# Kernel optimization log

Hardware: AMD Instinct MI355X
Metric: run time of the kernel (lower is better)

The kernel has to match this reference:

```python
import jax, jax.numpy as jnp
import numpy as np

B, T, E, H = 4, 2048, 1024, 16
D = E // H  # head dim = 64


def setup_inputs() -> dict:
    key = jax.random.key(0)
    k1, k2, k3 = jax.random.split(key, 3)
    g = jax.random.normal(k1, (B, T, E), dtype=jnp.float32)
    W_lift = jax.random.normal(k2, (2 * E, E), dtype=jnp.float32) * (1.0 / np.sqrt(E))
    W_proj = jax.random.normal(k3, (H, H), dtype=jnp.float32) * (1.0 / np.sqrt(H))
    return {"g": g, "W_lift": W_lift, "W_proj": W_proj}


def reference(g, W_lift, W_proj):
    b, t, e = g.shape
    h, d = H, e // H
    # lift: Linear(E, 2E, bias=False) -> split into q, k
    qk = jnp.einsum('bte,fe->btf', g, W_lift)  # (B, T, 2E)
    q, k = qk[..., :e], qk[..., e:]
    q = q.reshape(b, t, h, d).transpose(0, 2, 1, 3)  # (B, H, T, D)
    k = k.reshape(b, t, h, d).transpose(0, 2, 1, 3)  # (B, H, T, D)
    # unscaled causal scores
    a = jnp.einsum('bhqd,bhkd->bhqk', q, k)  # (B, H, T, T)
    causal = jnp.tril(jnp.ones((t, t), dtype=bool))
    a = jnp.where(causal[None, None], a, -jnp.inf)
    # masked logsumexp over key dim -> (B, H, T)
    lse = jax.scipy.special.logsumexp(a, axis=-1)
    out = lse.transpose(0, 2, 1)  # (B, T, H)
    out = jnp.einsum('bth,gh->btg', out, W_proj)  # proj Linear(H, H)
    out = out.sum(axis=2)  # (B, T)
    return out.reshape(-1, out.shape[-1])
```

## Files before the change

kernel.cpp:

```cpp
#include <hip/hip_runtime.h>
#include <hip/hip_bf16.h>

#define B_ 4
#define T_ 2048
#define E_ 1024
#define H_ 16
#define D_ 64
#define Mtot 8192
#define N2 2048
#define K_ 1024
#define PS_ (B_ * H_ * T_)
#define NKT 16
#define LOG2E 1.4426950408889634f

typedef __attribute__((ext_vector_type(8))) short short8;
typedef __attribute__((ext_vector_type(4))) float f32x4;
using bf16 = __hip_bfloat16;

__device__ __forceinline__ void async_copy16(const void* g, void* l) {
  __builtin_amdgcn_global_load_lds(
      (const __attribute__((address_space(1))) unsigned int*)g,
      (__attribute__((address_space(3))) unsigned int*)l, 16, 0, 0);
}

__global__ void cast_f32_to_bf16(const float* __restrict__ in, ushort* __restrict__ out, int n4) {
  int stride = gridDim.x * blockDim.x;
  for (int i = blockIdx.x * blockDim.x + threadIdx.x; i < n4; i += stride) {
    float4 v = reinterpret_cast<const float4*>(in)[i];
    bf16 a = __float2bfloat16(v.x), b = __float2bfloat16(v.y);
    bf16 c = __float2bfloat16(v.z), d = __float2bfloat16(v.w);
    ushort4 o = make_ushort4(*(ushort*)&a, *(ushort*)&b, *(ushort*)&c, *(ushort*)&d);
    reinterpret_cast<ushort4*>(out)[i] = o;
  }
}

#define MFMA_BF16(a, b, c) __builtin_amdgcn_mfma_f32_16x16x32_bf16(a, b, c, 0, 0, 0)

__launch_bounds__(512, 2)
__global__ void lift_gemm(const bf16* __restrict__ A, const bf16* __restrict__ Bm,
                          bf16* __restrict__ qh, bf16* __restrict__ kh) {
  __shared__ __align__(16) char sL[8][16384];
  const int bid = blockIdx.x;
  const int swz = ((bid & 7) << 5) | (bid >> 3);
  const int m0 = (swz >> 3) * 256;
  const int n0 = (swz & 7) * 256;
  const int tid = threadIdx.x;
  const int lane = tid & 63, w = tid >> 6;
  const int wm = w >> 2, wn = w & 3;
  const int lr = lane & 15, lg = lane >> 4;

  f32x4 acc[8][4];
#pragma unroll
  for (int i = 0; i < 8; ++i)
#pragma unroll
    for (int j = 0; j < 4; ++j) acc[i][j] = (f32x4)(0.0f);

  auto stage_half = [&](int slot, const bf16* gsrc, int Rbase, int kcol) {
#pragma unroll
    for (int it = 0; it < 2; ++it) {
      const int o = ((it * 512 + tid) << 4);
      const int lin = o ^ (((o >> 7) & 7) << 4);
      const int r = lin >> 7, cb = lin & 127;
      async_copy16((const char*)gsrc + ((size_t)(Rbase + r) * K_ + kcol) * 2 + cb,
                   &sL[slot][o]);
    }
  };
  auto rd = [&](int slot, int row, int khalf) -> short8 {
    int off = (row << 7) + (khalf << 6) + (lg << 4);
    off ^= (row & 7) << 4;
    return *(const short8*)&sL[slot][off];
  };

  stage_half(0, A, m0, 0);
  stage_half(1, A, m0 + 128, 0);
  stage_half(2, Bm, n0, 0);
  stage_half(3, Bm, n0 + 128, 0);

  short8 af[4][2], bf0[2][2], bf1[2][2];

  for (int kt = 0; kt < NKT; ++kt) {
    const int cb = (kt & 1) << 2;
    const int nb = cb ^ 4;
    const int kcol = (kt + 1) * 64;
    const int aslot = cb + wm;
    const int bslot = cb + 2 + (wn >> 1);
    const int brow = (wn & 1) * 64;

    if (kt + 1 < NKT) {
      stage_half(nb + 0, A, m0, kcol);
      stage_half(nb + 1, A, m0 + 128, kcol);
      asm volatile("s_waitcnt vmcnt(4)" ::: "memory");
    } else {
      asm volatile("s_waitcnt vmcnt(0)" ::: "memory");
    }
    __builtin_amdgcn_sched_barrier(0);
    __builtin_amdgcn_s_barrier();
#pragma unroll
    for (int i = 0; i < 4; ++i) {
      af[i][0] = rd(aslot, i * 16 + lr, 0);
      af[i][1] = rd(aslot, i * 16 + lr, 1);
    }
#pragma unroll
    for (int j = 0; j < 2; ++j) {
      bf0[j][0] = rd(bslot, brow + j * 16 + lr, 0);
      bf0[j][1] = rd(bslot, brow + j * 16 + lr, 1);
    }
    __builtin_amdgcn_s_setprio(1);
#pragma unroll
    for (int i = 0; i < 4; ++i)
#pragma unroll
      for (int j = 0; j < 2; ++j) {
        acc[i][j] = MFMA_BF16(af[i][0], bf0[j][0], acc[i][j]);
        acc[i][j] = MFMA_BF16(af[i][1], bf0[j][1], acc[i][j]);
      }
    __builtin_amdgcn_s_setprio(0);
    __builtin_amdgcn_sched_barrier(0);
    __builtin_amdgcn_s_barrier();

    if (kt + 1 < NKT) {
      stage_half(nb + 2, Bm, n0, kcol);
      stage_half(nb + 3, Bm, n0 + 128, kcol);
    }
#pragma unroll
    for (int j = 0; j < 2; ++j) {
      bf1[j][0] = rd(bslot, brow + (j + 2) * 16 + lr, 0);
      bf1[j][1] = rd(bslot, brow + (j + 2) * 16 + lr, 1);
    }
    __builtin_amdgcn_sched_barrier(0);
    __builtin_amdgcn_s_barrier();
    __builtin_amdgcn_s_setprio(1);
#pragma unroll
    for (int i = 0; i < 4; ++i)
#pragma unroll
      for (int j = 0; j < 2; ++j) {
        acc[i][j + 2] = MFMA_BF16(af[i][0], bf1[j][0], acc[i][j + 2]);
        acc[i][j + 2] = MFMA_BF16(af[i][1], bf1[j][1], acc[i][j + 2]);
      }
    __builtin_amdgcn_s_setprio(0);
    __builtin_amdgcn_sched_barrier(0);
    __builtin_amdgcn_s_barrier();

#pragma unroll
    for (int i = 0; i < 4; ++i) {
      af[i][0] = rd(aslot, (i + 4) * 16 + lr, 0);
      af[i][1] = rd(aslot, (i + 4) * 16 + lr, 1);
    }
    __builtin_amdgcn_sched_barrier(0);
    __builtin_amdgcn_s_barrier();
    __builtin_amdgcn_s_setprio(1);
#pragma unroll
    for (int i = 0; i < 4; ++i)
#pragma unroll
      for (int j = 0; j < 2; ++j) {
        acc[i + 4][j] = MFMA_BF16(af[i][0], bf0[j][0], acc[i + 4][j]);
        acc[i + 4][j] = MFMA_BF16(af[i][1], bf0[j][1], acc[i + 4][j]);
      }
    __builtin_amdgcn_s_setprio(0);
    __builtin_amdgcn_sched_barrier(0);
    __builtin_amdgcn_s_barrier();

    __builtin_amdgcn_s_setprio(1);
#pragma unroll
    for (int i = 0; i < 4; ++i)
#pragma unroll
      for (int j = 0; j < 2; ++j) {
        acc[i + 4][j + 2] = MFMA_BF16(af[i][0], bf1[j][0], acc[i + 4][j + 2]);
        acc[i + 4][j + 2] = MFMA_BF16(af[i][1], bf1[j][1], acc[i + 4][j + 2]);
      }
    __builtin_amdgcn_s_setprio(0);
    __builtin_amdgcn_sched_barrier(0);
    __builtin_amdgcn_s_barrier();
  }

  const float qscale = (n0 < E_) ? LOG2E : 1.0f;
#pragma unroll
  for (int mi = 0; mi < 8; ++mi) {
#pragma unroll
    for (int ni = 0; ni < 4; ++ni) {
#pragma unroll
      for (int r = 0; r < 4; ++r) {
        int m = m0 + wm * 128 + mi * 16 + lg * 4 + r;
        int f = n0 + wn * 64 + ni * 16 + lr;
        bf16 bv = __float2bfloat16(acc[mi][ni][r] * qscale);
        int b = m >> 11, t = m & (T_ - 1);
        int hh = (f & (E_ - 1)) >> 6, d = f & (D_ - 1);
        bf16* dst = (f < E_) ? qh : kh;
        dst[((((size_t)b * H_ + hh) * T_) + t) * D_ + d] = bv;
      }
    }
  }
}

#define LSE_QT 128

__launch_bounds__(256)
__global__ void attn_lse(const bf16* __restrict__ qh, const bf16* __restrict__ kh,
                         float* __restrict__ psum) {
  __shared__ __align__(16) char sK[2][8192];
  const int bid = blockIdx.x;
  const int qt = 15 - (bid >> 8);
  const int rem = bid & 255;
  const int bh = rem >> 2;
  const int s = rem & 3;
  const int tid = threadIdx.x;
  const int lane = tid & 63, w = tid >> 6;
  const int lr = lane & 15, lg = lane >> 4;
  const int qbase = qt * LSE_QT + w * 32;

  const bf16* qp = qh + ((size_t)bh * T_ + qbase) * D_;
  short8 qf[2][2];
#pragma unroll
  for (int f = 0; f < 2; ++f)
#pragma unroll
    for (int h = 0; h < 2; ++h)
      qf[f][h] = *(const short8*)&qp[(size_t)(f * 16 + lr) * D_ + h * 32 + lg * 8];

  float l[2][4];
#pragma unroll
  for (int f = 0; f < 2; ++f)
#pragma unroll
    for (int r = 0; r < 4; ++r) l[f][r] = 0.0f;

  const char* kbase = (const char*)(kh + (size_t)bh * T_ * D_);
  const int nfullw = qbase >> 6;
  const int maxk = 2 * qt + 1;
  const int nt = (s <= maxk) ? ((maxk - s) >> 2) + 1 : 0;

#define STAGE_K(bi, kt_)                                                      \
  do {                                                                        \
    const char* kp_ = kbase + (size_t)(kt_) * (64 * D_ * 2);                  \
    _Pragma("unroll") for (int it = 0; it < 2; ++it) {                        \
      const int o = ((w * 2 + it) << 10) | (lane << 4);                       \
      const int lin = o ^ (((o >> 7) & 7) << 4);                              \
      async_copy16(kp_ + lin, (char*)&sK[bi][0] + ((w * 2 + it) << 10));      \
    }                                                                         \
  } while (0)

  auto krd = [&](const char* kb, int row, int khalf) -> short8 {
    int off = (row << 7) + (khalf << 6) + (lg << 4);
    off ^= (row & 7) << 4;
    return *(const short8*)(kb + off);
  };

  int cur = 0;
  if (nt > 0) STAGE_K(0, s);
  for (int i = 0; i < nt; ++i) {
    if (i + 1 < nt) {
      STAGE_K(cur ^ 1, s + 4 * (i + 1));
      asm volatile("s_waitcnt vmcnt(2)" ::: "memory");
    } else {
      asm volatile("s_waitcnt vmcnt(0)" ::: "memory");
    }
    __builtin_amdgcn_sched_barrier(0);
    __builtin_amdgcn_s_barrier();

    const int kt = s + 4 * i;
    if (kt <= nfullw) {
      const char* kb = &sK[cur][0];
      short8 kf[4][2];
#pragma unroll
      for (int j = 0; j < 4; ++j) {
        kf[j][0] = krd(kb, j * 16 + lr, 0);
        kf[j][1] = krd(kb, j * 16 + lr, 1);
      }
      f32x4 sc[2][4];
#pragma unroll
      for (int f = 0; f < 2; ++f)
#pragma unroll
        for (int j = 0; j < 4; ++j) sc[f][j] = (f32x4)(0.0f);
#pragma unroll
      for (int j = 0; j < 4; ++j) {
        sc[0][j] = MFMA_BF16(qf[0][0], kf[j][0], sc[0][j]);
        sc[0][j] = MFMA_BF16(qf[0][1], kf[j][1], sc[0][j]);
        sc[1][j] = MFMA_BF16(qf[1][0], kf[j][0], sc[1][j]);
        sc[1][j] = MFMA_BF16(qf[1][1], kf[j][1], sc[1][j]);
      }
      if (kt < nfullw) {
#pragma unroll
        for (int f = 0; f < 2; ++f)
#pragma unroll
          for (int j = 0; j < 4; ++j)
#pragma unroll
            for (int r = 0; r < 4; ++r)
              l[f][r] += __builtin_amdgcn_exp2f(sc[f][j][r]);
      } else {
#pragma unroll
        for (int f = 0; f < 2; ++f)
#pragma unroll
          for (int j = 0; j < 4; ++j)
#pragma unroll
            for (int r = 0; r < 4; ++r) {
              int qrow = qbase + f * 16 + lg * 4 + r;
              int key = kt * 64 + j * 16 + lr;
              float a = (key <= qrow) ? sc[f][j][r] : -INFINITY;
              l[f][r] += __builtin_amdgcn_exp2f(a);
            }
      }
    }
    __builtin_amdgcn_sched_barrier(0);
    __builtin_amdgcn_s_barrier();
    cur ^= 1;
  }

#pragma unroll
  for (int f = 0; f < 2; ++f)
#pragma unroll
    for (int r = 0; r < 4; ++r) {
      float v = l[f][r];
      v += __shfl_xor(v, 1);
      v += __shfl_xor(v, 2);
      v += __shfl_xor(v, 4);
      v += __shfl_xor(v, 8);
      if (lr == 0)
        psum[(size_t)s * PS_ + (size_t)bh * T_ + qbase + f * 16 + lg * 4 + r] = v;
    }
}

__global__ void proj_out(const float* __restrict__ psum, const float* __restrict__ Wp,
                         float* __restrict__ out) {
  __shared__ float cw[H_];
  int tid = threadIdx.x;
  if (tid < H_) {
    float s = 0.0f;
    for (int g = 0; g < H_; ++g) s += Wp[g * H_ + tid];
    cw[tid] = s;
  }
  __syncthreads();
  int idx = blockIdx.x * blockDim.x + tid;
  int b = idx >> 11, t = idx & (T_ - 1);
  float acc = 0.0f;
#pragma unroll
  for (int h = 0; h < H_; ++h) {
    size_t base = ((size_t)(b * H_ + h) * T_) + t;
    float v = psum[base] + psum[PS_ + base] + psum[2 * (size_t)PS_ + base] +
              psum[3 * (size_t)PS_ + base];
    acc += __logf(v) * cw[h];
  }
  out[idx] = acc;
}

extern "C" void kernel_launch(void* const* d_in, const int* in_sizes, int n_in,
                              void* d_out, int out_size, void* d_ws, size_t ws_size,
                              hipStream_t stream) {
  (void)in_sizes; (void)n_in; (void)out_size; (void)ws_size;
  const float* g  = (const float*)d_in[0];
  const float* Wl = (const float*)d_in[1];
  const float* Wp = (const float*)d_in[2];
  float* out = (float*)d_out;

  char* ws = (char*)d_ws;
  size_t off = 0;
  bf16* g_bf  = (bf16*)(ws + off); off += (size_t)Mtot * K_ * 2;
  bf16* wl_bf = (bf16*)(ws + off); off += (size_t)N2 * K_ * 2;
  bf16* qh    = (bf16*)(ws + off); off += (size_t)B_ * H_ * T_ * D_ * 2;
  bf16* kh    = (bf16*)(ws + off); off += (size_t)B_ * H_ * T_ * D_ * 2;
  float* psum = (float*)(ws + off);

  cast_f32_to_bf16<<<2048, 256, 0, stream>>>(g,  (ushort*)g_bf,  (Mtot * K_) / 4);
  cast_f32_to_bf16<<<512,  256, 0, stream>>>(Wl, (ushort*)wl_bf, (N2 * K_) / 4);

  lift_gemm<<<256, 512, 0, stream>>>(g_bf, wl_bf, qh, kh);

  attn_lse<<<4096, 256, 0, stream>>>(qh, kh, psum);

  proj_out<<<(B_ * T_) / 256, 256, 0, stream>>>(psum, Wp, out);
}
```

Before: 88.35 us.

## Simplify GEMM k-loop to two MFMA phases with all prefetches issued upfront

Restructures the lift GEMM main loop. All four next-tile async loads (A and B halves) are now issued at the top of the iteration, followed by a single wait and barrier. Each wave then loads its whole B fragment set and computes in two MFMA phases instead of four, which drops most of the per-iteration barriers. The cost is more live registers for fragments and less interleaving of loads with MFMA work.

```diff
diff --git a/kernel.cpp b/kernel.cpp
--- a/kernel.cpp
+++ b/kernel.cpp
@@ -76,8 +76,6 @@
   stage_half(2, Bm, n0, 0);
   stage_half(3, Bm, n0 + 128, 0);
 
-  short8 af[4][2], bf0[2][2], bf1[2][2];
-
   for (int kt = 0; kt < NKT; ++kt) {
     const int cb = (kt & 1) << 2;
     const int nb = cb ^ 4;
@@ -89,83 +87,48 @@
     if (kt + 1 < NKT) {
       stage_half(nb + 0, A, m0, kcol);
       stage_half(nb + 1, A, m0 + 128, kcol);
-      asm volatile("s_waitcnt vmcnt(4)" ::: "memory");
+      stage_half(nb + 2, Bm, n0, kcol);
+      stage_half(nb + 3, Bm, n0 + 128, kcol);
+      asm volatile("s_waitcnt vmcnt(8)" ::: "memory");
     } else {
       asm volatile("s_waitcnt vmcnt(0)" ::: "memory");
     }
     __builtin_amdgcn_sched_barrier(0);
     __builtin_amdgcn_s_barrier();
+
+    short8 bf[4][2], af[4][2];
+#pragma unroll
+    for (int j = 0; j < 4; ++j) {
+      bf[j][0] = rd(bslot, brow + j * 16 + lr, 0);
+      bf[j][1] = rd(bslot, brow + j * 16 + lr, 1);
+    }
 #pragma unroll
     for (int i = 0; i < 4; ++i) {
       af[i][0] = rd(aslot, i * 16 + lr, 0);
       af[i][1] = rd(aslot, i * 16 + lr, 1);
     }
-#pragma unroll
-    for (int j = 0; j < 2; ++j) {
-      bf0[j][0] = rd(bslot, brow + j * 16 + lr, 0);
-      bf0[j][1] = rd(bslot, brow + j * 16 + lr, 1);
-    }
     __builtin_amdgcn_s_setprio(1);
 #pragma unroll
     for (int i = 0; i < 4; ++i)
 #pragma unroll
-      for (int j = 0; j < 2; ++j) {
-        acc[i][j] = MFMA_BF16(af[i][0], bf0[j][0], acc[i][j]);
-        acc[i][j] = MFMA_BF16(af[i][1], bf0[j][1], acc[i][j]);
+      for (int j = 0; j < 4; ++j) {
+        acc[i][j] = MFMA_BF16(af[i][0], bf[j][0], acc[i][j]);
+        acc[i][j] = MFMA_BF16(af[i][1], bf[j][1], acc[i][j]);
       }
     __builtin_amdgcn_s_setprio(0);
-    __builtin_amdgcn_sched_barrier(0);
-    __builtin_amdgcn_s_barrier();
-
-    if (kt + 1 < NKT) {
-      stage_half(nb + 2, Bm, n0, kcol);
-      stage_half(nb + 3, Bm, n0 + 128, kcol);
-    }
-#pragma unroll
-    for (int j = 0; j < 2; ++j) {
-      bf1[j][0] = rd(bslot, brow + (j + 2) * 16 + lr, 0);
-      bf1[j][1] = rd(bslot, brow + (j + 2) * 16 + lr, 1);
-    }
-    __builtin_amdgcn_sched_barrier(0);
-    __builtin_amdgcn_s_barrier();
+    short8 ah[4][2];
+#pragma unroll
+    for (int i = 0; i < 4; ++i) {
+      ah[i][0] = rd(aslot, (i + 4) * 16 + lr, 0);
+      ah[i][1] = rd(aslot, (i + 4) * 16 + lr, 1);
+    }
     __builtin_amdgcn_s_setprio(1);
 #pragma unroll
     for (int i = 0; i < 4; ++i)
 #pragma unroll
-      for (int j = 0; j < 2; ++j) {
-        acc[i][j + 2] = MFMA_BF16(af[i][0], bf1[j][0], acc[i][j + 2]);
-        acc[i][j + 2] = MFMA_BF16(af[i][1], bf1[j][1], acc[i][j + 2]);
-      }
-    __builtin_amdgcn_s_setprio(0);
-    __builtin_amdgcn_sched_barrier(0);
-    __builtin_amdgcn_s_barrier();
-
-#pragma unroll
-    for (int i = 0; i < 4; ++i) {
-      af[i][0] = rd(aslot, (i + 4) * 16 + lr, 0);
-      af[i][1] = rd(aslot, (i + 4) * 16 + lr, 1);
-    }
-    __builtin_amdgcn_sched_barrier(0);
-    __builtin_amdgcn_s_barrier();
-    __builtin_amdgcn_s_setprio(1);
-#pragma unroll
-    for (int i = 0; i < 4; ++i)
-#pragma unroll
-      for (int j = 0; j < 2; ++j) {
-        acc[i + 4][j] = MFMA_BF16(af[i][0], bf0[j][0], acc[i + 4][j]);
-        acc[i + 4][j] = MFMA_BF16(af[i][1], bf0[j][1], acc[i + 4][j]);
-      }
-    __builtin_amdgcn_s_setprio(0);
-    __builtin_amdgcn_sched_barrier(0);
-    __builtin_amdgcn_s_barrier();
-
-    __builtin_amdgcn_s_setprio(1);
-#pragma unroll
-    for (int i = 0; i < 4; ++i)
-#pragma unroll
-      for (int j = 0; j < 2; ++j) {
-        acc[i + 4][j + 2] = MFMA_BF16(af[i][0], bf1[j][0], acc[i + 4][j + 2]);
-        acc[i + 4][j + 2] = MFMA_BF16(af[i][1], bf1[j][1], acc[i + 4][j + 2]);
+      for (int j = 0; j < 4; ++j) {
+        acc[i + 4][j] = MFMA_BF16(ah[i][0], bf[j][0], acc[i + 4][j]);
+        acc[i + 4][j] = MFMA_BF16(ah[i][1], bf[j][1], acc[i + 4][j]);
       }
     __builtin_amdgcn_s_setprio(0);
     __builtin_amdgcn_sched_barrier(0);
```

Result: no change. 89.25 us (+1.0%).

## Deepen lift GEMM prefetch to two K-tiles ahead with staggered staging

Applied to the files above, without the earlier changes.

Restructures the lift GEMM main loop to preload two K-tiles up front and process two tiles per iteration. Each LDS slot is refilled as soon as its last reader is done, spread across the MFMA phases, with vmcnt waits retuned to match. The aim is to hide more global-load latency behind MFMA work. The cost is more complex slot-reuse logic and wait counts that, if wrong, could cause races or stalls.

```diff
diff --git a/kernel.cpp b/kernel.cpp
--- a/kernel.cpp
+++ b/kernel.cpp
@@ -48,6 +48,7 @@
   const int lane = tid & 63, w = tid >> 6;
   const int wm = w >> 2, wn = w & 3;
   const int lr = lane & 15, lg = lane >> 4;
+  const int brow = (wn & 1) * 64;
 
   f32x4 acc[8][4];
 #pragma unroll
@@ -75,101 +76,129 @@
   stage_half(1, A, m0 + 128, 0);
   stage_half(2, Bm, n0, 0);
   stage_half(3, Bm, n0 + 128, 0);
-
-  short8 af[4][2], bf0[2][2], bf1[2][2];
-
-  for (int kt = 0; kt < NKT; ++kt) {
-    const int cb = (kt & 1) << 2;
-    const int nb = cb ^ 4;
-    const int kcol = (kt + 1) * 64;
-    const int aslot = cb + wm;
-    const int bslot = cb + 2 + (wn >> 1);
-    const int brow = (wn & 1) * 64;
-
-    if (kt + 1 < NKT) {
-      stage_half(nb + 0, A, m0, kcol);
-      stage_half(nb + 1, A, m0 + 128, kcol);
-      asm volatile("s_waitcnt vmcnt(4)" ::: "memory");
-    } else {
-      asm volatile("s_waitcnt vmcnt(0)" ::: "memory");
-    }
-    __builtin_amdgcn_sched_barrier(0);
-    __builtin_amdgcn_s_barrier();
-#pragma unroll
-    for (int i = 0; i < 4; ++i) {
-      af[i][0] = rd(aslot, i * 16 + lr, 0);
-      af[i][1] = rd(aslot, i * 16 + lr, 1);
-    }
-#pragma unroll
-    for (int j = 0; j < 2; ++j) {
-      bf0[j][0] = rd(bslot, brow + j * 16 + lr, 0);
-      bf0[j][1] = rd(bslot, brow + j * 16 + lr, 1);
-    }
-    __builtin_amdgcn_s_setprio(1);
-#pragma unroll
-    for (int i = 0; i < 4; ++i)
+  stage_half(4, A, m0, 64);
+  stage_half(5, A, m0 + 128, 64);
+  stage_half(6, Bm, n0, 64);
+  stage_half(7, Bm, n0 + 128, 64);
+  asm volatile("s_waitcnt vmcnt(0)" ::: "memory");
+  __builtin_amdgcn_sched_barrier(0);
+  __builtin_amdgcn_s_barrier();
+
+  short8 al[4][2], ah[4][2], bl[2][2], bh[2][2];
+
+  for (int it = 0; it < 8; ++it) {
+    const bool pf = (it < 7);
+    const int kcA = (2 * it + 2) * 64;
+    const int kcB = (2 * it + 3) * 64;
+
+#pragma unroll
+    for (int d = 0; d < 2; ++d) {
+      const int as = d * 4 + wm;
+      const int bs = d * 4 + 2 + (wn >> 1);
+
+#pragma unroll
+      for (int i = 0; i < 4; ++i) {
+        al[i][0] = rd(as, i * 16 + lr, 0);
+        al[i][1] = rd(as, i * 16 + lr, 1);
+      }
 #pragma unroll
       for (int j = 0; j < 2; ++j) {
-        acc[i][j] = MFMA_BF16(af[i][0], bf0[j][0], acc[i][j]);
-        acc[i][j] = MFMA_BF16(af[i][1], bf0[j][1], acc[i][j]);
-      }
-    __builtin_amdgcn_s_setprio(0);
-    __builtin_amdgcn_sched_barrier(0);
-    __builtin_amdgcn_s_barrier();
-
-    if (kt + 1 < NKT) {
-      stage_half(nb + 2, Bm, n0, kcol);
-      stage_half(nb + 3, Bm, n0 + 128, kcol);
-    }
-#pragma unroll
-    for (int j = 0; j < 2; ++j) {
-      bf1[j][0] = rd(bslot, brow + (j + 2) * 16 + lr, 0);
-      bf1[j][1] = rd(bslot, brow + (j + 2) * 16 + lr, 1);
-    }
-    __builtin_amdgcn_sched_barrier(0);
-    __builtin_amdgcn_s_barrier();
-    __builtin_amdgcn_s_setprio(1);
-#pragma unroll
-    for (int i = 0; i < 4; ++i)
+        bl[j][0] = rd(bs, brow + j * 16 + lr, 0);
+        bl[j][1] = rd(bs, brow + j * 16 + lr, 1);
+      }
+      __builtin_amdgcn_sched_barrier(0);
+      __builtin_amdgcn_s_barrier();
+      __builtin_amdgcn_s_setprio(1);
+#pragma unroll
+      for (int i = 0; i < 4; ++i)
+#pragma unroll
+        for (int j = 0; j < 2; ++j) {
+          acc[i][j] = MFMA_BF16(al[i][0], bl[j][0], acc[i][j]);
+          acc[i][j] = MFMA_BF16(al[i][1], bl[j][1], acc[i][j]);
+        }
+      __builtin_amdgcn_s_setprio(0);
+      __builtin_amdgcn_sched_barrier(0);
+      __builtin_amdgcn_s_barrier();
+
 #pragma unroll
       for (int j = 0; j < 2; ++j) {
-        acc[i][j + 2] = MFMA_BF16(af[i][0], bf1[j][0], acc[i][j + 2]);
-        acc[i][j + 2] = MFMA_BF16(af[i][1], bf1[j][1], acc[i][j + 2]);
-      }
-    __builtin_amdgcn_s_setprio(0);
-    __builtin_amdgcn_sched_barrier(0);
-    __builtin_amdgcn_s_barrier();
-
-#pragma unroll
-    for (int i = 0; i < 4; ++i) {
-      af[i][0] = rd(aslot, (i + 4) * 16 + lr, 0);
-      af[i][1] = rd(aslot, (i + 4) * 16 + lr, 1);
-    }
-    __builtin_amdgcn_sched_barrier(0);
-    __builtin_amdgcn_s_barrier();
-    __builtin_amdgcn_s_setprio(1);
-#pragma unroll
-    for (int i = 0; i < 4; ++i)
-#pragma unroll
-      for (int j = 0; j < 2; ++j) {
-        acc[i + 4][j] = MFMA_BF16(af[i][0], bf0[j][0], acc[i + 4][j]);
-        acc[i + 4][j] = MFMA_BF16(af[i][1], bf0[j][1], acc[i + 4][j]);
-      }
-    __builtin_amdgcn_s_setprio(0);
-    __builtin_amdgcn_sched_barrier(0);
-    __builtin_amdgcn_s_barrier();
-
-    __builtin_amdgcn_s_setprio(1);
-#pragma unroll
-    for (int i = 0; i < 4; ++i)
-#pragma unroll
-      for (int j = 0; j < 2; ++j) {
-        acc[i + 4][j + 2] = MFMA_BF16(af[i][0], bf1[j][0], acc[i + 4][j + 2]);
-        acc[i + 4][j + 2] = MFMA_BF16(af[i][1], bf1[j][1], acc[i + 4][j + 2]);
-      }
-    __builtin_amdgcn_s_setprio(0);
-    __builtin_amdgcn_sched_barrier(0);
-    __builtin_amdgcn_s_barrier();
+        bh[j][0] = rd(bs, brow + (j + 2) * 16 + lr, 0);
+        bh[j][1] = rd(bs, brow + (j + 2) * 16 + lr, 1);
+      }
+      __builtin_amdgcn_sched_barrier(0);
+      __builtin_amdgcn_s_barrier();
+      __builtin_amdgcn_s_setprio(1);
+#pragma unroll
+      for (int i = 0; i < 4; ++i)
+#pragma unroll
+        for (int j = 0; j < 2; ++j) {
+          acc[i][j + 2] = MFMA_BF16(al[i][0], bh[j][0], acc[i][j + 2]);
+          acc[i][j + 2] = MFMA_BF16(al[i][1], bh[j][1], acc[i][j + 2]);
+        }
+      __builtin_amdgcn_s_setprio(0);
+      __builtin_amdgcn_sched_barrier(0);
+      __builtin_amdgcn_s_barrier();
+
+#pragma unroll
+      for (int i = 0; i < 4; ++i) {
+        ah[i][0] = rd(as, (i + 4) * 16 + lr, 0);
+        ah[i][1] = rd(as, (i + 4) * 16 + lr, 1);
+      }
+      if (pf) {
+        if (d == 0) {
+          stage_half(2, Bm, n0, kcA);
+          stage_half(3, Bm, n0 + 128, kcA);
+        } else {
+          stage_half(6, Bm, n0, kcB);
+          stage_half(7, Bm, n0 + 128, kcB);
+        }
+      }
+      __builtin_amdgcn_sched_barrier(0);
+      __builtin_amdgcn_s_barrier();
+      __builtin_amdgcn_s_setprio(1);
+#pragma unroll
+      for (int i = 0; i < 4; ++i)
+#pragma unroll
+        for (int j = 0; j < 2; ++j) {
+          acc[i + 4][j] = MFMA_BF16(ah[i][0], bl[j][0], acc[i + 4][j]);
+          acc[i + 4][j] = MFMA_BF16(ah[i][1], bl[j][1], acc[i + 4][j]);
+        }
+      __builtin_amdgcn_s_setprio(0);
+      __builtin_amdgcn_sched_barrier(0);
+      __builtin_amdgcn_s_barrier();
+
+      if (d == 0) {
+        if (pf) {
+          stage_half(0, A, m0, kcA);
+          asm volatile("s_waitcnt vmcnt(6)" ::: "memory");
+        } else {
+          asm volatile("s_waitcnt vmcnt(0)" ::: "memory");
+        }
+      } else {
+        if (pf) {
+          stage_half(4, A, m0, kcB);
+          stage_half(5, A, m0 + 128, kcB);
+          asm volatile("s_waitcnt vmcnt(8)" ::: "memory");
+        } else {
+          asm volatile("s_waitcnt vmcnt(0)" ::: "memory");
+        }
+      }
+      __builtin_amdgcn_sched_barrier(0);
+      __builtin_amdgcn_s_barrier();
+      __builtin_amdgcn_s_setprio(1);
+#pragma unroll
+      for (int i = 0; i < 4; ++i)
+#pragma unroll
+        for (int j = 0; j < 2; ++j) {
+          acc[i + 4][j + 2] = MFMA_BF16(ah[i][0], bh[j][0], acc[i + 4][j + 2]);
+          acc[i + 4][j + 2] = MFMA_BF16(ah[i][1], bh[j][1], acc[i + 4][j + 2]);
+        }
+      __builtin_amdgcn_s_setprio(0);
+      __builtin_amdgcn_sched_barrier(0);
+      __builtin_amdgcn_s_barrier();
+
+      if (d == 0 && pf) stage_half(1, A, m0 + 128, kcA);
+    }
   }
 
   const float qscale = (n0 < E_) ? LOG2E : 1.0f;
```

Result: slower. 126.7 us (+43.5%).

## Merge cast kernels and shrink attention query tiles to 64 rows

Applied to the files above, without the earlier changes.

The two f32-to-bf16 cast launches are merged into one kernel that covers both tensors, removing one launch. The attention logsumexp kernel moves from 128-row query tiles with 4 waves to 64-row tiles with 2 waves, doubling the grid to 8192 blocks. Each wave now stages twice as much K per tile, and the per-wave causal skip check is dropped because every wave in a block shares the same diagonal tile. This aims for finer causal load balancing and less wasted masked work, but each K tile loaded into shared memory is now reused by fewer query rows.

```diff
diff --git a/kernel.cpp b/kernel.cpp
--- a/kernel.cpp
+++ b/kernel.cpp
@@ -23,14 +23,20 @@
       (__attribute__((address_space(3))) unsigned int*)l, 16, 0, 0);
 }
 
-__global__ void cast_f32_to_bf16(const float* __restrict__ in, ushort* __restrict__ out, int n4) {
+__global__ void cast_both(const float* __restrict__ g, const float* __restrict__ wl,
+                          ushort* __restrict__ og, ushort* __restrict__ owl) {
+  const int n4g = (Mtot * K_) / 4;
+  const int tot = n4g + (N2 * K_) / 4;
   int stride = gridDim.x * blockDim.x;
-  for (int i = blockIdx.x * blockDim.x + threadIdx.x; i < n4; i += stride) {
-    float4 v = reinterpret_cast<const float4*>(in)[i];
+  for (int i = blockIdx.x * blockDim.x + threadIdx.x; i < tot; i += stride) {
+    const float4* src = (i < n4g) ? &reinterpret_cast<const float4*>(g)[i]
+                                  : &reinterpret_cast<const float4*>(wl)[i - n4g];
+    ushort4* dst = (i < n4g) ? &reinterpret_cast<ushort4*>(og)[i]
+                             : &reinterpret_cast<ushort4*>(owl)[i - n4g];
+    float4 v = *src;
     bf16 a = __float2bfloat16(v.x), b = __float2bfloat16(v.y);
     bf16 c = __float2bfloat16(v.z), d = __float2bfloat16(v.w);
-    ushort4 o = make_ushort4(*(ushort*)&a, *(ushort*)&b, *(ushort*)&c, *(ushort*)&d);
-    reinterpret_cast<ushort4*>(out)[i] = o;
+    *dst = make_ushort4(*(ushort*)&a, *(ushort*)&b, *(ushort*)&c, *(ushort*)&d);
   }
 }
 
@@ -191,21 +197,19 @@
   }
 }
 
-#define LSE_QT 128
-
-__launch_bounds__(256)
+__launch_bounds__(128)
 __global__ void attn_lse(const bf16* __restrict__ qh, const bf16* __restrict__ kh,
                          float* __restrict__ psum) {
   __shared__ __align__(16) char sK[2][8192];
   const int bid = blockIdx.x;
-  const int qt = 15 - (bid >> 8);
+  const int qt = 31 - (bid >> 8);
   const int rem = bid & 255;
   const int bh = rem >> 2;
   const int s = rem & 3;
   const int tid = threadIdx.x;
   const int lane = tid & 63, w = tid >> 6;
   const int lr = lane & 15, lg = lane >> 4;
-  const int qbase = qt * LSE_QT + w * 32;
+  const int qbase = qt * 64 + w * 32;
 
   const bf16* qp = qh + ((size_t)bh * T_ + qbase) * D_;
   short8 qf[2][2];
@@ -222,17 +226,16 @@
     for (int r = 0; r < 4; ++r) l[f][r] = 0.0f;
 
   const char* kbase = (const char*)(kh + (size_t)bh * T_ * D_);
-  const int nfullw = qbase >> 6;
-  const int maxk = 2 * qt + 1;
-  const int nt = (s <= maxk) ? ((maxk - s) >> 2) + 1 : 0;
+  const int nfullw = qt;
+  const int nt = (s <= qt) ? ((qt - s) >> 2) + 1 : 0;
 
 #define STAGE_K(bi, kt_)                                                      \
   do {                                                                        \
     const char* kp_ = kbase + (size_t)(kt_) * (64 * D_ * 2);                  \
-    _Pragma("unroll") for (int it = 0; it < 2; ++it) {                        \
-      const int o = ((w * 2 + it) << 10) | (lane << 4);                       \
+    _Pragma("unroll") for (int it = 0; it < 4; ++it) {                        \
+      const int o = ((w * 4 + it) << 10) | (lane << 4);                       \
       const int lin = o ^ (((o >> 7) & 7) << 4);                              \
-      async_copy16(kp_ + lin, (char*)&sK[bi][0] + ((w * 2 + it) << 10));      \
+      async_copy16(kp_ + lin, (char*)&sK[bi][0] + o);                         \
     }                                                                         \
   } while (0)
 
@@ -247,7 +250,7 @@
   for (int i = 0; i < nt; ++i) {
     if (i + 1 < nt) {
       STAGE_K(cur ^ 1, s + 4 * (i + 1));
-      asm volatile("s_waitcnt vmcnt(2)" ::: "memory");
+      asm volatile("s_waitcnt vmcnt(4)" ::: "memory");
     } else {
       asm volatile("s_waitcnt vmcnt(0)" ::: "memory");
     }
@@ -255,7 +258,7 @@
     __builtin_amdgcn_s_barrier();
 
     const int kt = s + 4 * i;
-    if (kt <= nfullw) {
+    {
       const char* kb = &sK[cur][0];
       short8 kf[4][2];
 #pragma unroll
@@ -356,12 +359,11 @@
   bf16* kh    = (bf16*)(ws + off); off += (size_t)B_ * H_ * T_ * D_ * 2;
   float* psum = (float*)(ws + off);
 
-  cast_f32_to_bf16<<<2048, 256, 0, stream>>>(g,  (ushort*)g_bf,  (Mtot * K_) / 4);
-  cast_f32_to_bf16<<<512,  256, 0, stream>>>(Wl, (ushort*)wl_bf, (N2 * K_) / 4);
+  cast_both<<<2560, 256, 0, stream>>>(g, Wl, (ushort*)g_bf, (ushort*)wl_bf);
 
   lift_gemm<<<256, 512, 0, stream>>>(g_bf, wl_bf, qh, kh);
 
-  attn_lse<<<4096, 256, 0, stream>>>(qh, kh, psum);
+  attn_lse<<<8192, 128, 0, stream>>>(qh, kh, psum);
 
   proj_out<<<(B_ * T_) / 256, 256, 0, stream>>>(psum, Wp, out);
 }
```

New measurement: 90.06 us. Within noise of the previous version (+1.9%).
